# Performance work log

Measured on AMD Instinct MI355X. Metric: run time of the kernel, lower is better.

## Reference

```python
import jax, jax.numpy as jnp
import numpy as np

C = 64      # input_channels
H = 448     # height (= conv groups)
W = 608     # width
K = 32      # stage_1_classes
B = 2       # batch


def lrelu(v):
    # F.leaky_relu default negative_slope=0.01
    return jnp.where(v >= 0, v, 0.01 * v)


def setup_inputs() -> dict:
    key = jax.random.key(0)
    ks = jax.random.split(key, 9)
    s = jnp.float32(0.05)
    return {
        "x":  jax.random.normal(ks[0], (B, C, H, W), jnp.float32),
        # grouped 1x1 convs, groups=H -> per-row [C_out, C_in] matrices
        "W1": jax.random.normal(ks[1], (H, C, C), jnp.float32) * s,
        "b1": jax.random.normal(ks[2], (H, C), jnp.float32) * s,
        "W2": jax.random.normal(ks[3], (H, C, C), jnp.float32) * s,
        "b2": jax.random.normal(ks[4], (H, C), jnp.float32) * s,
        "W3": jax.random.normal(ks[5], (H, K, C), jnp.float32) * s,
        "b3": jax.random.normal(ks[6], (H, K), jnp.float32) * s,
        # RefCondMul: per-class linear table [H*K classes, C in, 2 out]
        "Wr": jax.random.normal(ks[7], (H * K, C, 2), jnp.float32) * s,
        "br": jax.random.normal(ks[8], (H * K, 2), jnp.float32) * s,
    }


def reference(x, W1, b1, W2, b2, W3, b3, Wr, br):
    b = x.shape[0]
    # x: [B,C,H,W] -> [B,H,C,W]  (transpose(1,2) then grouped-by-row 1x1 convs)
    x1 = jnp.transpose(x, (0, 2, 1, 3))
    x1 = lrelu(jnp.einsum('hoc,bhcw->bhow', W1, x1) + b1[None, :, :, None])
    x1 = lrelu(jnp.einsum('hoc,bhcw->bhow', W2, x1) + b2[None, :, :, None])
    cls = lrelu(jnp.einsum('hkc,bhcw->bhkw', W3, x1) + b3[None, :, :, None])  # [B,H,K,W]
    inds = jnp.argmax(cls, axis=2)                         # [B,H,W]
    inds = inds + (jnp.arange(H, dtype=inds.dtype) * K)[None, :, None]  # + offset*K
    flat = inds.reshape(-1)                                # [B*H*W]
    # RefCondMul: per-pixel class-conditioned linear on original features
    x2 = jnp.transpose(x, (0, 2, 3, 1)).reshape(-1, C)     # [B*H*W, C]
    reg = lrelu(jnp.einsum('nc,nco->no', x2, Wr[flat]) + br[flat])  # [B*H*W, 2]
    reg = reg.reshape(b, H, W, 2)
    inds3 = flat.reshape(b, H, W).astype(jnp.float32)
    xpos = (inds3 + reg[..., 0]) * (1.0 / K)
    mask = lrelu(reg[..., 1])
    return xpos, mask
```

## Files before the change

kernel.cpp:

```cpp
#include <hip/hip_runtime.h>

namespace {

constexpr int C   = 64;
constexpr int H   = 448;
constexpr int Wd  = 608;
constexpr int K   = 32;
constexpr int B   = 2;
constexpr int PIX = 128;
constexpr int NTILE = 5;
constexpr int NBLK  = H * NTILE;

constexpr size_t W2T_BYTES = (size_t)H * C * C * sizeof(float);

__device__ __forceinline__ float lrelu(float v) {
    return v >= 0.0f ? v : 0.01f * v;
}

__global__ __launch_bounds__(256)
void transpose_w2(const float* __restrict__ W2, float* __restrict__ W2T) {
    __shared__ float t[C][C + 1];
    const int h = blockIdx.x;
    const float* __restrict__ in  = W2  + (size_t)h * C * C;
    float* __restrict__       op  = W2T + (size_t)h * C * C;
    const int tid = threadIdx.x;
#pragma unroll
    for (int k = 0; k < (C * C) / 256; ++k) {
        const int idx = tid + k * 256;
        t[idx >> 6][idx & 63] = in[idx];
    }
    __syncthreads();
#pragma unroll
    for (int k = 0; k < (C * C) / 256; ++k) {
        const int idx = tid + k * 256;
        op[idx] = t[idx & 63][idx >> 6];
    }
}

template <bool USE_WT>
__global__ __launch_bounds__(256, 3)
void reg1stage_kernel(const float* __restrict__ x,
                      const float* __restrict__ W1, const float* __restrict__ b1,
                      const float* __restrict__ W2orT, const float* __restrict__ b2,
                      const float* __restrict__ W3, const float* __restrict__ b3,
                      const float* __restrict__ Wr, const float* __restrict__ br,
                      float* __restrict__ out)
{
    __shared__ float sW1[C * C];
    __shared__ float sW2[C * C];
    __shared__ float sW3[K * C];

    const int tid = threadIdx.x;

    const int wg   = blockIdx.x;
    const int swz  = (wg & 7) * (NBLK / 8) + (wg >> 3);
    const int h    = swz / NTILE;
    const int tile = swz - NTILE * h;

    const int wave = tid >> 6;
    const int lane = tid & 63;
    const int col  = lane & 31;
    const int half = lane >> 5;
    const int cb   = half * 32;
    const int w    = tile * PIX + wave * 32 + col;
    const bool valid = (w < Wd);
    const int wc   = valid ? w : (Wd - 1);

    const size_t HW = (size_t)H * Wd;
    const float* __restrict__ W1h = W1    + (size_t)h * C * C;
    const float* __restrict__ W2h = W2orT + (size_t)h * C * C;
    const float* __restrict__ W3h = W3    + (size_t)h * K * C;
    const float* __restrict__ b1h = b1 + (size_t)h * C;
    const float* __restrict__ b2h = b2 + (size_t)h * C;
    const float* __restrict__ b3h = b3 + (size_t)h * K;

    {
        const float4* __restrict__ g1 = reinterpret_cast<const float4*>(W1h);
        const float4* __restrict__ g2 = reinterpret_cast<const float4*>(W2h);
        const float4* __restrict__ g3 = reinterpret_cast<const float4*>(W3h);
        float4* s1 = reinterpret_cast<float4*>(sW1);
        float4* s2 = reinterpret_cast<float4*>(sW2);
        float4* s3 = reinterpret_cast<float4*>(sW3);
#pragma unroll
        for (int r = 0; r < 4; ++r) s1[tid + 256 * r] = g1[tid + 256 * r];
#pragma unroll
        for (int r = 0; r < 4; ++r) s2[tid + 256 * r] = g2[tid + 256 * r];
#pragma unroll
        for (int r = 0; r < 2; ++r) s3[tid + 256 * r] = g3[tid + 256 * r];
    }

    float xv0[32], xv1[32];
    {
        const float* __restrict__ x0 = x + (((size_t)0 * C + cb) * H + h) * Wd + wc;
        const float* __restrict__ x1 = x + (((size_t)1 * C + cb) * H + h) * Wd + wc;
#pragma unroll
        for (int c = 0; c < 32; ++c) {
            xv0[c] = x0[(size_t)c * HW];
            xv1[c] = x1[(size_t)c * HW];
        }
    }

    float a20[32], a21[32];
    {
        const float4* __restrict__ bv = reinterpret_cast<const float4*>(b2h + cb);
#pragma unroll
        for (int i = 0; i < 8; ++i) {
            const float4 t = bv[i];
            a20[4*i+0] = t.x; a20[4*i+1] = t.y; a20[4*i+2] = t.z; a20[4*i+3] = t.w;
            a21[4*i+0] = t.x; a21[4*i+1] = t.y; a21[4*i+2] = t.z; a21[4*i+3] = t.w;
        }
    }

    __syncthreads();

#pragma unroll 1
    for (int c = 0; c < C; ++c) {
        float p0 = 0.0f, q0 = 0.0f, p1 = 0.0f, q1 = 0.0f;
#pragma unroll
        for (int i = 0; i < 8; ++i) {
            const float4 wv = *reinterpret_cast<const float4*>(&sW1[c * C + cb + 4 * i]);
            p0 = fmaf(wv.x, xv0[4*i+0], p0);
            q0 = fmaf(wv.y, xv0[4*i+1], q0);
            p0 = fmaf(wv.z, xv0[4*i+2], p0);
            q0 = fmaf(wv.w, xv0[4*i+3], q0);
            p1 = fmaf(wv.x, xv1[4*i+0], p1);
            q1 = fmaf(wv.y, xv1[4*i+1], q1);
            p1 = fmaf(wv.z, xv1[4*i+2], p1);
            q1 = fmaf(wv.w, xv1[4*i+3], q1);
        }
        float s0 = p0 + q0;
        float s1 = p1 + q1;
        s0 += __shfl_xor(s0, 32);
        s1 += __shfl_xor(s1, 32);
        const float b1c  = b1h[c];
        const float a1c0 = lrelu(b1c + s0);
        const float a1c1 = lrelu(b1c + s1);

        if constexpr (USE_WT) {
#pragma unroll
            for (int i = 0; i < 8; ++i) {
                const float4 wv = *reinterpret_cast<const float4*>(&sW2[c * C + cb + 4 * i]);
                a20[4*i+0] = fmaf(wv.x, a1c0, a20[4*i+0]);
                a20[4*i+1] = fmaf(wv.y, a1c0, a20[4*i+1]);
                a20[4*i+2] = fmaf(wv.z, a1c0, a20[4*i+2]);
                a20[4*i+3] = fmaf(wv.w, a1c0, a20[4*i+3]);
                a21[4*i+0] = fmaf(wv.x, a1c1, a21[4*i+0]);
                a21[4*i+1] = fmaf(wv.y, a1c1, a21[4*i+1]);
                a21[4*i+2] = fmaf(wv.z, a1c1, a21[4*i+2]);
                a21[4*i+3] = fmaf(wv.w, a1c1, a21[4*i+3]);
            }
        } else {
#pragma unroll
            for (int o = 0; o < 32; ++o) {
                const float wv = sW2[(cb + o) * C + c];
                a20[o] = fmaf(wv, a1c0, a20[o]);
                a21[o] = fmaf(wv, a1c1, a21[o]);
            }
        }
    }
#pragma unroll
    for (int o = 0; o < 32; ++o) { a20[o] = lrelu(a20[o]); a21[o] = lrelu(a21[o]); }

    float best0 = -3.402823466e38f, best1 = -3.402823466e38f;
    int   bi0 = 0, bi1 = 0;
#pragma unroll 1
    for (int kt = 0; kt < K / 4; ++kt) {
        float s0[4] = {0,0,0,0};
        float s1[4] = {0,0,0,0};
#pragma unroll
        for (int i = 0; i < 8; ++i) {
#pragma unroll
            for (int j = 0; j < 4; ++j) {
                const float4 wv =
                    *reinterpret_cast<const float4*>(&sW3[(kt*4 + j) * C + cb + 4 * i]);
                s0[j] = fmaf(wv.x, a20[4*i+0], s0[j]);
                s0[j] = fmaf(wv.y, a20[4*i+1], s0[j]);
                s0[j] = fmaf(wv.z, a20[4*i+2], s0[j]);
                s0[j] = fmaf(wv.w, a20[4*i+3], s0[j]);
                s1[j] = fmaf(wv.x, a21[4*i+0], s1[j]);
                s1[j] = fmaf(wv.y, a21[4*i+1], s1[j]);
                s1[j] = fmaf(wv.z, a21[4*i+2], s1[j]);
                s1[j] = fmaf(wv.w, a21[4*i+3], s1[j]);
            }
        }
#pragma unroll
        for (int j = 0; j < 4; ++j) {
            const float bj = b3h[kt*4 + j];
            const float t0 = s0[j] + __shfl_xor(s0[j], 32) + bj;
            const float t1 = s1[j] + __shfl_xor(s1[j], 32) + bj;
            if (t0 > best0) { best0 = t0; bi0 = kt*4 + j; }
            if (t1 > best1) { best1 = t1; bi1 = kt*4 + j; }
        }
    }

    const int flat0 = h * K + bi0;
    const int flat1 = h * K + bi1;
    const float4* __restrict__ wr0 =
        reinterpret_cast<const float4*>(Wr + (size_t)flat0 * C * 2) + (cb >> 1);
    const float4* __restrict__ wr1 =
        reinterpret_cast<const float4*>(Wr + (size_t)flat1 * C * 2) + (cb >> 1);
    float f00 = 0.0f, f01 = 0.0f, f10 = 0.0f, f11 = 0.0f;
#pragma unroll
    for (int j = 0; j < 16; ++j) {
        const float4 w0 = wr0[j];
        f00 = fmaf(xv0[2*j+0], w0.x, f00);
        f01 = fmaf(xv0[2*j+0], w0.y, f01);
        f00 = fmaf(xv0[2*j+1], w0.z, f00);
        f01 = fmaf(xv0[2*j+1], w0.w, f01);
        const float4 w1 = wr1[j];
        f10 = fmaf(xv1[2*j+0], w1.x, f10);
        f11 = fmaf(xv1[2*j+0], w1.y, f11);
        f10 = fmaf(xv1[2*j+1], w1.z, f10);
        f11 = fmaf(xv1[2*j+1], w1.w, f11);
    }
    f00 += __shfl_xor(f00, 32);
    f01 += __shfl_xor(f01, 32);
    f10 += __shfl_xor(f10, 32);
    f11 += __shfl_xor(f11, 32);

    const float r00 = lrelu(f00 + br[2 * flat0 + 0]);
    const float r01 = lrelu(f01 + br[2 * flat0 + 1]);
    const float r10 = lrelu(f10 + br[2 * flat1 + 0]);
    const float r11 = lrelu(f11 + br[2 * flat1 + 1]);

    if (valid && half == 0) {
        const size_t HWall = (size_t)B * H * Wd;
        const size_t o0 = ((size_t)0 * H + h) * Wd + w;
        const size_t o1 = ((size_t)1 * H + h) * Wd + w;
        out[o0]         = ((float)flat0 + r00) * (1.0f / K);
        out[o1]         = ((float)flat1 + r10) * (1.0f / K);
        out[HWall + o0] = lrelu(r01);
        out[HWall + o1] = lrelu(r11);
    }
}

}

extern "C" void kernel_launch(void* const* d_in, const int* in_sizes, int n_in,
                              void* d_out, int out_size, void* d_ws, size_t ws_size,
                              hipStream_t stream) {
    const float* x  = (const float*)d_in[0];
    const float* W1 = (const float*)d_in[1];
    const float* b1 = (const float*)d_in[2];
    const float* W2 = (const float*)d_in[3];
    const float* b2 = (const float*)d_in[4];
    const float* W3 = (const float*)d_in[5];
    const float* b3 = (const float*)d_in[6];
    const float* Wr = (const float*)d_in[7];
    const float* br = (const float*)d_in[8];
    float* out = (float*)d_out;

    dim3 grid(NBLK);
    dim3 block(256);

    if (ws_size >= W2T_BYTES) {
        float* W2T = (float*)d_ws;
        hipLaunchKernelGGL(transpose_w2, dim3(H), dim3(256), 0, stream, W2, W2T);
        hipLaunchKernelGGL((reg1stage_kernel<true>), grid, block, 0, stream,
                           x, W1, b1, W2T, b2, W3, b3, Wr, br, out);
    } else {
        hipLaunchKernelGGL((reg1stage_kernel<false>), grid, block, 0, stream,
                           x, W1, b1, W2, b2, W3, b3, Wr, br, out);
    }
}
```

Baseline: 358.5 us.

## Split channel reduction across four lane quarters with two pixels per lane

Changes the thread mapping so each lane handles 16 channels and two pixel columns per batch (four pixel streams) instead of 32 channels and one column, using a two-step shuffle reduction. This halves per-lane register arrays and doubles reuse of each shared-memory weight load across pixels. It also drops the W3 shared-memory copy, reading W3 directly from global, and reloads x from global in the RefCondMul stage instead of keeping it in registers. The cost is extra shuffles, more global reads of x and W3, and more uncoalesced 16-wide column accesses.

```diff
diff --git a/kernel.cpp b/kernel.cpp
--- a/kernel.cpp
+++ b/kernel.cpp
@@ -2,12 +2,12 @@
 
 namespace {
 
-constexpr int C   = 64;
-constexpr int H   = 448;
-constexpr int Wd  = 608;
-constexpr int K   = 32;
-constexpr int B   = 2;
-constexpr int PIX = 128;
+constexpr int C    = 64;
+constexpr int H    = 448;
+constexpr int Wd   = 608;
+constexpr int K    = 32;
+constexpr int B    = 2;
+constexpr int COLS = 128;
 constexpr int NTILE = 5;
 constexpr int NBLK  = H * NTILE;
 
@@ -48,7 +48,6 @@
 {
     __shared__ float sW1[C * C];
     __shared__ float sW2[C * C];
-    __shared__ float sW3[K * C];
 
     const int tid = threadIdx.x;
 
@@ -59,12 +58,15 @@
 
     const int wave = tid >> 6;
     const int lane = tid & 63;
-    const int col  = lane & 31;
-    const int half = lane >> 5;
-    const int cb   = half * 32;
-    const int w    = tile * PIX + wave * 32 + col;
-    const bool valid = (w < Wd);
-    const int wc   = valid ? w : (Wd - 1);
+    const int cpos = lane & 15;
+    const int qtr  = lane >> 4;
+    const int cb   = qtr * 16;
+    const int w0   = tile * COLS + wave * 32 + cpos;
+    const int w1   = w0 + 16;
+    const bool v0  = (w0 < Wd);
+    const bool v1  = (w1 < Wd);
+    const int wc0  = v0 ? w0 : (Wd - 1);
+    const int wc1  = v1 ? w1 : (Wd - 1);
 
     const size_t HW = (size_t)H * Wd;
     const float* __restrict__ W1h = W1    + (size_t)h * C * C;
@@ -74,163 +76,207 @@
     const float* __restrict__ b2h = b2 + (size_t)h * C;
     const float* __restrict__ b3h = b3 + (size_t)h * K;
 
+    const float* __restrict__ xb0 = x + (((size_t)0 * C + cb) * H + h) * Wd;
+    const float* __restrict__ xb1 = x + (((size_t)1 * C + cb) * H + h) * Wd;
+
     {
         const float4* __restrict__ g1 = reinterpret_cast<const float4*>(W1h);
         const float4* __restrict__ g2 = reinterpret_cast<const float4*>(W2h);
-        const float4* __restrict__ g3 = reinterpret_cast<const float4*>(W3h);
         float4* s1 = reinterpret_cast<float4*>(sW1);
         float4* s2 = reinterpret_cast<float4*>(sW2);
-        float4* s3 = reinterpret_cast<float4*>(sW3);
 #pragma unroll
         for (int r = 0; r < 4; ++r) s1[tid + 256 * r] = g1[tid + 256 * r];
 #pragma unroll
         for (int r = 0; r < 4; ++r) s2[tid + 256 * r] = g2[tid + 256 * r];
-#pragma unroll
-        for (int r = 0; r < 2; ++r) s3[tid + 256 * r] = g3[tid + 256 * r];
-    }
-
-    float xv0[32], xv1[32];
+    }
+
+    float a200[16], a201[16], a210[16], a211[16];
+#pragma unroll
+    for (int j = 0; j < 16; ++j) {
+        const float bb = b2h[cb + j];
+        a200[j] = bb; a201[j] = bb; a210[j] = bb; a211[j] = bb;
+    }
+
+    __syncthreads();
+
     {
-        const float* __restrict__ x0 = x + (((size_t)0 * C + cb) * H + h) * Wd + wc;
-        const float* __restrict__ x1 = x + (((size_t)1 * C + cb) * H + h) * Wd + wc;
-#pragma unroll
-        for (int c = 0; c < 32; ++c) {
-            xv0[c] = x0[(size_t)c * HW];
-            xv1[c] = x1[(size_t)c * HW];
-        }
-    }
-
-    float a20[32], a21[32];
-    {
-        const float4* __restrict__ bv = reinterpret_cast<const float4*>(b2h + cb);
-#pragma unroll
-        for (int i = 0; i < 8; ++i) {
-            const float4 t = bv[i];
-            a20[4*i+0] = t.x; a20[4*i+1] = t.y; a20[4*i+2] = t.z; a20[4*i+3] = t.w;
-            a21[4*i+0] = t.x; a21[4*i+1] = t.y; a21[4*i+2] = t.z; a21[4*i+3] = t.w;
-        }
-    }
-
-    __syncthreads();
+        float x00[16], x01[16], x10[16], x11[16];
+#pragma unroll
+        for (int ch = 0; ch < 16; ++ch) {
+            const size_t o = (size_t)ch * HW;
+            x00[ch] = xb0[o + wc0];
+            x01[ch] = xb0[o + wc1];
+            x10[ch] = xb1[o + wc0];
+            x11[ch] = xb1[o + wc1];
+        }
 
 #pragma unroll 1
-    for (int c = 0; c < C; ++c) {
-        float p0 = 0.0f, q0 = 0.0f, p1 = 0.0f, q1 = 0.0f;
-#pragma unroll
-        for (int i = 0; i < 8; ++i) {
-            const float4 wv = *reinterpret_cast<const float4*>(&sW1[c * C + cb + 4 * i]);
-            p0 = fmaf(wv.x, xv0[4*i+0], p0);
-            q0 = fmaf(wv.y, xv0[4*i+1], q0);
-            p0 = fmaf(wv.z, xv0[4*i+2], p0);
-            q0 = fmaf(wv.w, xv0[4*i+3], q0);
-            p1 = fmaf(wv.x, xv1[4*i+0], p1);
-            q1 = fmaf(wv.y, xv1[4*i+1], q1);
-            p1 = fmaf(wv.z, xv1[4*i+2], p1);
-            q1 = fmaf(wv.w, xv1[4*i+3], q1);
-        }
-        float s0 = p0 + q0;
-        float s1 = p1 + q1;
-        s0 += __shfl_xor(s0, 32);
-        s1 += __shfl_xor(s1, 32);
-        const float b1c  = b1h[c];
-        const float a1c0 = lrelu(b1c + s0);
-        const float a1c1 = lrelu(b1c + s1);
-
-        if constexpr (USE_WT) {
-#pragma unroll
-            for (int i = 0; i < 8; ++i) {
-                const float4 wv = *reinterpret_cast<const float4*>(&sW2[c * C + cb + 4 * i]);
-                a20[4*i+0] = fmaf(wv.x, a1c0, a20[4*i+0]);
-                a20[4*i+1] = fmaf(wv.y, a1c0, a20[4*i+1]);
-                a20[4*i+2] = fmaf(wv.z, a1c0, a20[4*i+2]);
-                a20[4*i+3] = fmaf(wv.w, a1c0, a20[4*i+3]);
-                a21[4*i+0] = fmaf(wv.x, a1c1, a21[4*i+0]);
-                a21[4*i+1] = fmaf(wv.y, a1c1, a21[4*i+1]);
-                a21[4*i+2] = fmaf(wv.z, a1c1, a21[4*i+2]);
-                a21[4*i+3] = fmaf(wv.w, a1c1, a21[4*i+3]);
+        for (int c = 0; c < C; ++c) {
+            float p00 = 0.0f, p01 = 0.0f, p10 = 0.0f, p11 = 0.0f;
+#pragma unroll
+            for (int i = 0; i < 4; ++i) {
+                const float4 wv = *reinterpret_cast<const float4*>(&sW1[c * C + cb + 4 * i]);
+                p00 = fmaf(wv.x, x00[4*i+0], p00);
+                p00 = fmaf(wv.y, x00[4*i+1], p00);
+                p00 = fmaf(wv.z, x00[4*i+2], p00);
+                p00 = fmaf(wv.w, x00[4*i+3], p00);
+                p01 = fmaf(wv.x, x01[4*i+0], p01);
+                p01 = fmaf(wv.y, x01[4*i+1], p01);
+                p01 = fmaf(wv.z, x01[4*i+2], p01);
+                p01 = fmaf(wv.w, x01[4*i+3], p01);
+                p10 = fmaf(wv.x, x10[4*i+0], p10);
+                p10 = fmaf(wv.y, x10[4*i+1], p10);
+                p10 = fmaf(wv.z, x10[4*i+2], p10);
+                p10 = fmaf(wv.w, x10[4*i+3], p10);
+                p11 = fmaf(wv.x, x11[4*i+0], p11);
+                p11 = fmaf(wv.y, x11[4*i+1], p11);
+                p11 = fmaf(wv.z, x11[4*i+2], p11);
+                p11 = fmaf(wv.w, x11[4*i+3], p11);
             }
-        } else {
-#pragma unroll
-            for (int o = 0; o < 32; ++o) {
-                const float wv = sW2[(cb + o) * C + c];
-                a20[o] = fmaf(wv, a1c0, a20[o]);
-                a21[o] = fmaf(wv, a1c1, a21[o]);
+            p00 += __shfl_xor(p00, 16); p00 += __shfl_xor(p00, 32);
+            p01 += __shfl_xor(p01, 16); p01 += __shfl_xor(p01, 32);
+            p10 += __shfl_xor(p10, 16); p10 += __shfl_xor(p10, 32);
+            p11 += __shfl_xor(p11, 16); p11 += __shfl_xor(p11, 32);
+
+            const float b1c = b1h[c];
+            const float a0 = lrelu(b1c + p00);
+            const float a1 = lrelu(b1c + p01);
+            const float a2v = lrelu(b1c + p10);
+            const float a3 = lrelu(b1c + p11);
+
+            if constexpr (USE_WT) {
+#pragma unroll
+                for (int i = 0; i < 4; ++i) {
+                    const float4 wv = *reinterpret_cast<const float4*>(&sW2[c * C + cb + 4 * i]);
+                    a200[4*i+0] = fmaf(wv.x, a0, a200[4*i+0]);
+                    a200[4*i+1] = fmaf(wv.y, a0, a200[4*i+1]);
+                    a200[4*i+2] = fmaf(wv.z, a0, a200[4*i+2]);
+                    a200[4*i+3] = fmaf(wv.w, a0, a200[4*i+3]);
+                    a201[4*i+0] = fmaf(wv.x, a1, a201[4*i+0]);
+                    a201[4*i+1] = fmaf(wv.y, a1, a201[4*i+1]);
+                    a201[4*i+2] = fmaf(wv.z, a1, a201[4*i+2]);
+                    a201[4*i+3] = fmaf(wv.w, a1, a201[4*i+3]);
+                    a210[4*i+0] = fmaf(wv.x, a2v, a210[4*i+0]);
+                    a210[4*i+1] = fmaf(wv.y, a2v, a210[4*i+1]);
+                    a210[4*i+2] = fmaf(wv.z, a2v, a210[4*i+2]);
+                    a210[4*i+3] = fmaf(wv.w, a2v, a210[4*i+3]);
+                    a211[4*i+0] = fmaf(wv.x, a3, a211[4*i+0]);
+                    a211[4*i+1] = fmaf(wv.y, a3, a211[4*i+1]);
+                    a211[4*i+2] = fmaf(wv.z, a3, a211[4*i+2]);
+                    a211[4*i+3] = fmaf(wv.w, a3, a211[4*i+3]);
+                }
+            } else {
+#pragma unroll
+                for (int j = 0; j < 16; ++j) {
+                    const float wv = sW2[(cb + j) * C + c];
+                    a200[j] = fmaf(wv, a0,  a200[j]);
+                    a201[j] = fmaf(wv, a1,  a201[j]);
+                    a210[j] = fmaf(wv, a2v, a210[j]);
+                    a211[j] = fmaf(wv, a3,  a211[j]);
+                }
             }
         }
     }
-#pragma unroll
-    for (int o = 0; o < 32; ++o) { a20[o] = lrelu(a20[o]); a21[o] = lrelu(a21[o]); }
-
-    float best0 = -3.402823466e38f, best1 = -3.402823466e38f;
-    int   bi0 = 0, bi1 = 0;
+
+#pragma unroll
+    for (int j = 0; j < 16; ++j) {
+        a200[j] = lrelu(a200[j]); a201[j] = lrelu(a201[j]);
+        a210[j] = lrelu(a210[j]); a211[j] = lrelu(a211[j]);
+    }
+
+    float be00 = -3.402823466e38f, be01 = be00, be10 = be00, be11 = be00;
+    int   bi00 = 0, bi01 = 0, bi10 = 0, bi11 = 0;
 #pragma unroll 1
     for (int kt = 0; kt < K / 4; ++kt) {
-        float s0[4] = {0,0,0,0};
-        float s1[4] = {0,0,0,0};
-#pragma unroll
-        for (int i = 0; i < 8; ++i) {
-#pragma unroll
-            for (int j = 0; j < 4; ++j) {
-                const float4 wv =
-                    *reinterpret_cast<const float4*>(&sW3[(kt*4 + j) * C + cb + 4 * i]);
-                s0[j] = fmaf(wv.x, a20[4*i+0], s0[j]);
-                s0[j] = fmaf(wv.y, a20[4*i+1], s0[j]);
-                s0[j] = fmaf(wv.z, a20[4*i+2], s0[j]);
-                s0[j] = fmaf(wv.w, a20[4*i+3], s0[j]);
-                s1[j] = fmaf(wv.x, a21[4*i+0], s1[j]);
-                s1[j] = fmaf(wv.y, a21[4*i+1], s1[j]);
-                s1[j] = fmaf(wv.z, a21[4*i+2], s1[j]);
-                s1[j] = fmaf(wv.w, a21[4*i+3], s1[j]);
+        float s00[4] = {0,0,0,0}, s01[4] = {0,0,0,0};
+        float s10[4] = {0,0,0,0}, s11[4] = {0,0,0,0};
+#pragma unroll
+        for (int j = 0; j < 4; ++j) {
+            const float4* __restrict__ w3r =
+                reinterpret_cast<const float4*>(&W3h[(kt*4 + j) * C + cb]);
+#pragma unroll
+            for (int i = 0; i < 4; ++i) {
+                const float4 wv = w3r[i];
+                s00[j] = fmaf(wv.x, a200[4*i+0], s00[j]);
+                s00[j] = fmaf(wv.y, a200[4*i+1], s00[j]);
+                s00[j] = fmaf(wv.z, a200[4*i+2], s00[j]);
+                s00[j] = fmaf(wv.w, a200[4*i+3], s00[j]);
+                s01[j] = fmaf(wv.x, a201[4*i+0], s01[j]);
+                s01[j] = fmaf(wv.y, a201[4*i+1], s01[j]);
+                s01[j] = fmaf(wv.z, a201[4*i+2], s01[j]);
+                s01[j] = fmaf(wv.w, a201[4*i+3], s01[j]);
+                s10[j] = fmaf(wv.x, a210[4*i+0], s10[j]);
+                s10[j] = fmaf(wv.y, a210[4*i+1], s10[j]);
+                s10[j] = fmaf(wv.z, a210[4*i+2], s10[j]);
+                s10[j] = fmaf(wv.w, a210[4*i+3], s10[j]);
+                s11[j] = fmaf(wv.x, a211[4*i+0], s11[j]);
+                s11[j] = fmaf(wv.y, a211[4*i+1], s11[j]);
+                s11[j] = fmaf(wv.z, a211[4*i+2], s11[j]);
+                s11[j] = fmaf(wv.w, a211[4*i+3], s11[j]);
             }
         }
 #pragma unroll
         for (int j = 0; j < 4; ++j) {
             const float bj = b3h[kt*4 + j];
-            const float t0 = s0[j] + __shfl_xor(s0[j], 32) + bj;
-            const float t1 = s1[j] + __shfl_xor(s1[j], 32) + bj;
-            if (t0 > best0) { best0 = t0; bi0 = kt*4 + j; }
-            if (t1 > best1) { best1 = t1; bi1 = kt*4 + j; }
-        }
-    }
-
-    const int flat0 = h * K + bi0;
-    const int flat1 = h * K + bi1;
-    const float4* __restrict__ wr0 =
-        reinterpret_cast<const float4*>(Wr + (size_t)flat0 * C * 2) + (cb >> 1);
-    const float4* __restrict__ wr1 =
-        reinterpret_cast<const float4*>(Wr + (size_t)flat1 * C * 2) + (cb >> 1);
-    float f00 = 0.0f, f01 = 0.0f, f10 = 0.0f, f11 = 0.0f;
-#pragma unroll
-    for (int j = 0; j < 16; ++j) {
-        const float4 w0 = wr0[j];
-        f00 = fmaf(xv0[2*j+0], w0.x, f00);
-        f01 = fmaf(xv0[2*j+0], w0.y, f01);
-        f00 = fmaf(xv0[2*j+1], w0.z, f00);
-        f01 = fmaf(xv0[2*j+1], w0.w, f01);
-        const float4 w1 = wr1[j];
-        f10 = fmaf(xv1[2*j+0], w1.x, f10);
-        f11 = fmaf(xv1[2*j+0], w1.y, f11);
-        f10 = fmaf(xv1[2*j+1], w1.z, f10);
-        f11 = fmaf(xv1[2*j+1], w1.w, f11);
-    }
-    f00 += __shfl_xor(f00, 32);
-    f01 += __shfl_xor(f01, 32);
-    f10 += __shfl_xor(f10, 32);
-    f11 += __shfl_xor(f11, 32);
-
-    const float r00 = lrelu(f00 + br[2 * flat0 + 0]);
-    const float r01 = lrelu(f01 + br[2 * flat0 + 1]);
-    const float r10 = lrelu(f10 + br[2 * flat1 + 0]);
-    const float r11 = lrelu(f11 + br[2 * flat1 + 1]);
-
-    if (valid && half == 0) {
+            float t00 = s00[j]; t00 += __shfl_xor(t00, 16); t00 += __shfl_xor(t00, 32); t00 += bj;
+            float t01 = s01[j]; t01 += __shfl_xor(t01, 16); t01 += __shfl_xor(t01, 32); t01 += bj;
+            float t10 = s10[j]; t10 += __shfl_xor(t10, 16); t10 += __shfl_xor(t10, 32); t10 += bj;
+            float t11 = s11[j]; t11 += __shfl_xor(t11, 16); t11 += __shfl_xor(t11, 32); t11 += bj;
+            const int k = kt*4 + j;
+            if (t00 > be00) { be00 = t00; bi00 = k; }
+            if (t01 > be01) { be01 = t01; bi01 = k; }
+            if (t10 > be10) { be10 = t10; bi10 = k; }
+            if (t11 > be11) { be11 = t11; bi11 = k; }
+        }
+    }
+
+    const int fl00 = h * K + bi00, fl01 = h * K + bi01;
+    const int fl10 = h * K + bi10, fl11 = h * K + bi11;
+
+    float r0_00, r1_00, r0_01, r1_01, r0_10, r1_10, r0_11, r1_11;
+#pragma unroll
+    for (int p = 0; p < 4; ++p) {
+        const int   flat = (p == 0) ? fl00 : (p == 1) ? fl01 : (p == 2) ? fl10 : fl11;
+        const int   wcp  = (p & 1) ? wc1 : wc0;
+        const float* __restrict__ xb = (p < 2) ? xb0 : xb1;
+        const float* __restrict__ wrp = Wr + (size_t)flat * C * 2 + (size_t)cb * 2;
+        float f0 = 0.0f, f1 = 0.0f;
+#pragma unroll
+        for (int t = 0; t < 8; ++t) {
+            const float4 q = *reinterpret_cast<const float4*>(&wrp[4 * t]);
+            const float xa = xb[(size_t)(2*t+0) * HW + wcp];
+            const float xbv = xb[(size_t)(2*t+1) * HW + wcp];
+            f0 = fmaf(xa,  q.x, f0);
+            f1 = fmaf(xa,  q.y, f1);
+            f0 = fmaf(xbv, q.z, f0);
+            f1 = fmaf(xbv, q.w, f1);
+        }
+        f0 += __shfl_xor(f0, 16); f0 += __shfl_xor(f0, 32);
+        f1 += __shfl_xor(f1, 16); f1 += __shfl_xor(f1, 32);
+        const float r0 = lrelu(f0 + br[2 * flat + 0]);
+        const float r1 = lrelu(f1 + br[2 * flat + 1]);
+        if (p == 0)      { r0_00 = r0; r1_00 = r1; }
+        else if (p == 1) { r0_01 = r0; r1_01 = r1; }
+        else if (p == 2) { r0_10 = r0; r1_10 = r1; }
+        else             { r0_11 = r0; r1_11 = r1; }
+    }
+
+    if (qtr == 0) {
         const size_t HWall = (size_t)B * H * Wd;
-        const size_t o0 = ((size_t)0 * H + h) * Wd + w;
-        const size_t o1 = ((size_t)1 * H + h) * Wd + w;
-        out[o0]         = ((float)flat0 + r00) * (1.0f / K);
-        out[o1]         = ((float)flat1 + r10) * (1.0f / K);
-        out[HWall + o0] = lrelu(r01);
-        out[HWall + o1] = lrelu(r11);
+        const size_t rowb0 = ((size_t)0 * H + h) * Wd;
+        const size_t rowb1 = ((size_t)1 * H + h) * Wd;
+        if (v0) {
+            out[rowb0 + w0]         = ((float)fl00 + r0_00) * (1.0f / K);
+            out[HWall + rowb0 + w0] = lrelu(r1_00);
+            out[rowb1 + w0]         = ((float)fl10 + r0_10) * (1.0f / K);
+            out[HWall + rowb1 + w0] = lrelu(r1_10);
+        }
+        if (v1) {
+            out[rowb0 + w1]         = ((float)fl01 + r0_01) * (1.0f / K);
+            out[HWall + rowb0 + w1] = lrelu(r1_01);
+            out[rowb1 + w1]         = ((float)fl11 + r0_11) * (1.0f / K);
+            out[HWall + rowb1 + w1] = lrelu(r1_11);
+        }
     }
 }
 
```

Result: slower. 414.4 us (+15.6%).
